# Kernel optimization log

Measured on AMD Instinct MI355X. Metric: run time of the kernel, lower is better.

Reference implementation:

```python
import jax, jax.numpy as jnp
import numpy as np

EPS = 1e-5
BANDLIMIT = 0.5
STEP_SCALE = 1.0


def _ln(x, g, b):
    mu = jnp.mean(x, axis=-1, keepdims=True)
    var = jnp.mean(jnp.square(x - mu), axis=-1, keepdims=True)
    return (x - mu) * jax.lax.rsqrt(var + EPS) * g + b


def _s5(u, Lambda_re, Lambda_im, B_re, B_im, C_re, C_im, D, log_step):
    # u: [N, T, C]; diagonal S5 SSM with ZOH discretization and parallel scan.
    Lam = Lambda_re + 1j * Lambda_im                      # [P] complex
    Bm = B_re + 1j * B_im                                  # [P, C]
    Cm = C_re + 1j * C_im                                  # [C, P]
    step = STEP_SCALE * jnp.exp(log_step)                  # [P]
    Lam_bar = jnp.exp(Lam * step)                          # [P]
    B_bar = ((Lam_bar - 1.0) / Lam)[:, None] * Bm          # [P, C]
    # bandlimit mask on output projection (freqs use un-scaled step)
    freqs = jnp.exp(log_step) * jnp.abs(Lambda_im) / (2.0 * jnp.pi)
    Cm = Cm * jnp.where(freqs < BANDLIMIT * 0.5, 1.0, 0.0)[None, :]
    Bu = jnp.einsum('ntc,pc->ntp', u.astype(B_bar.dtype), B_bar)  # [N,T,P] complex
    A = jnp.broadcast_to(Lam_bar, Bu.shape)

    def op(e1, e2):
        a1, b1 = e1
        a2, b2 = e2
        return a2 * a1, a2 * b1 + b2

    _, xs = jax.lax.associative_scan(op, (A, Bu), axis=1)   # x_t = Lam_bar*x_{t-1} + B_bar u_t (x_0 = 0)
    y = jnp.einsum('ntp,cp->ntc', xs, Cm).real + u * D
    return y


def setup_inputs() -> dict:
    key = jax.random.key(0)
    ks = jax.random.split(key, 16)
    B, T, H, W = 2, 15, 192, 192
    C, P = 16, 16
    sC = 1.0 / np.sqrt(C)
    sP = 1.0 / np.sqrt(P)
    inp = {}
    inp['x'] = jax.random.normal(ks[0], (B, T, H, W), dtype=jnp.float32)
    # input_proj: Linear(1, C)
    inp['w_in'] = jax.random.normal(ks[1], (C,), dtype=jnp.float32)
    inp['b_in'] = jnp.zeros((C,), dtype=jnp.float32)
    # S5Block attn_norm
    inp['attn_gamma'] = jnp.ones((C,), dtype=jnp.float32)
    inp['attn_beta'] = jnp.zeros((C,), dtype=jnp.float32)
    # S5 SSM parameters (stable: Re(Lambda) < 0)
    inp['Lambda_re'] = -jax.random.uniform(ks[2], (P,), jnp.float32, 0.1, 1.0)
    inp['Lambda_im'] = jnp.pi * jnp.arange(P, dtype=jnp.float32)
    inp['B_re'] = sC * jax.random.normal(ks[3], (P, C), dtype=jnp.float32)
    inp['B_im'] = sC * jax.random.normal(ks[4], (P, C), dtype=jnp.float32)
    inp['C_re'] = sP * jax.random.normal(ks[5], (C, P), dtype=jnp.float32)
    inp['C_im'] = sP * jax.random.normal(ks[6], (C, P), dtype=jnp.float32)
    inp['D'] = jax.random.normal(ks[7], (C,), dtype=jnp.float32)
    inp['log_step'] = jax.random.uniform(ks[8], (P,), jnp.float32, np.log(1e-3), np.log(0.1))
    # S5Block FFN (GEGLU, ff_mult=1.0, no bias)
    inp['ff_gamma'] = jnp.ones((C,), dtype=jnp.float32)
    inp['ff_beta'] = jnp.zeros((C,), dtype=jnp.float32)
    inp['W_enc'] = sC * jax.random.normal(ks[9], (2 * C, C), dtype=jnp.float32)
    inp['W_dec'] = sC * jax.random.normal(ks[10], (C, C), dtype=jnp.float32)
    # output_proj: LayerNorm(C) + Linear(C, C)
    inp['out_gamma'] = jnp.ones((C,), dtype=jnp.float32)
    inp['out_beta'] = jnp.zeros((C,), dtype=jnp.float32)
    inp['W_out'] = sC * jax.random.normal(ks[11], (C, C), dtype=jnp.float32)
    inp['b_out'] = jnp.zeros((C,), dtype=jnp.float32)
    return inp


def reference(x, w_in, b_in, attn_gamma, attn_beta, Lambda_re, Lambda_im,
              B_re, B_im, C_re, C_im, D, log_step,
              ff_gamma, ff_beta, W_enc, W_dec,
              out_gamma, out_beta, W_out, b_out):
    b, t, h, w = x.shape
    C = w_in.shape[0]
    # (b t h w) -> (b h w) t 1 -> Linear(1, C)
    u = jnp.transpose(x, (0, 2, 3, 1)).reshape(b * h * w, t)          # [N, T]
    u = u[:, :, None] * w_in + b_in                                     # [N, T, C]
    # --- S5Block ---
    fx = _ln(u, attn_gamma, attn_beta)
    s5_out = _s5(fx, Lambda_re, Lambda_im, B_re, B_im, C_re, C_im, D, log_step)
    z = jax.nn.gelu(s5_out, approximate=False) + fx
    fx2 = _ln(z, ff_gamma, ff_beta)
    enc = fx2 @ W_enc.T                                                 # [N, T, 2C]
    a, g = enc[..., :C], enc[..., C:]
    z2 = (a * jax.nn.gelu(g, approximate=False)) @ W_dec.T + fx2
    # aggregation = 'last'
    agg = z2[:, -1, :]                                                  # [N, C]
    # output_proj
    out = _ln(agg, out_gamma, out_beta) @ W_out.T + b_out               # [N, C]
    y = jnp.transpose(out.reshape(b, h, w, C), (0, 3, 1, 2))            # [B, C, H, W]
    return y
```

## Files before the change

### kernel.cpp

```cpp
#include <hip/hip_runtime.h>
#include <math.h>

#define HW_TOT 36864
#define T_LEN  15
#define NSEQ   73728
#define NBLK   576

#define OFF_F1    4
#define OFF_F2    20
#define OFF_F3    36
#define OFF_D     52
#define OFF_G3    68
#define OFF_G12   84
#define OFF_WENC  596
#define OFF_WDEC  1108
#define OFF_WOUT  1364
#define OFF_FFG   1620
#define OFF_FFB   1636
#define OFF_OG    1652
#define OFF_OB    1668
#define OFF_BOUT  1684
#define SM_N      1700

__device__ __forceinline__ float gelu_exact(float x){
  float ax = fabsf(x) * 0.7071067811865476f;
  float t  = 1.0f / (1.0f + 0.3275911f * ax);
  float poly = t*(0.254829592f + t*(-0.284496736f + t*(1.421413741f +
               t*(-1.453152027f + t*1.061405429f))));
  float er = 1.0f - poly * __expf(-ax*ax);
  er = copysignf(er, x);
  return 0.5f * x * (1.0f + er);
}

__global__ void __launch_bounds__(64) ssm_setup(
    const float* __restrict__ w_in, const float* __restrict__ b_in,
    const float* __restrict__ ag,   const float* __restrict__ ab,
    const float* __restrict__ Lre,  const float* __restrict__ Lim,
    const float* __restrict__ Bre,  const float* __restrict__ Bim,
    const float* __restrict__ Cre,  const float* __restrict__ Cim,
    const float* __restrict__ Dv,   const float* __restrict__ ls,
    const float* __restrict__ ffg,  const float* __restrict__ ffb,
    const float* __restrict__ Wenc, const float* __restrict__ Wdec,
    const float* __restrict__ og,   const float* __restrict__ ob,
    const float* __restrict__ Wout, const float* __restrict__ bout,
    float* __restrict__ ws)
{
  __shared__ float U1r[240], U1i[240], U2r[240], U2i[240];
  __shared__ float Cr[256], Ci[256], Qr[16], Qi[16];
  const int tid = threadIdx.x;

  float mw = 0.f, mb = 0.f;
  for (int c = 0; c < 16; ++c){ mw += w_in[c]; mb += b_in[c]; }
  mw *= 0.0625f; mb *= 0.0625f;
  float Saa = 0.f, Sad = 0.f, Sdd = 0.f;
  for (int c = 0; c < 16; ++c){
    float a = w_in[c]-mw, d = b_in[c]-mb;
    Saa += a*a; Sad += a*d; Sdd += d*d;
  }
  Saa *= 0.0625f; Sad *= 0.0625f; Sdd *= 0.0625f;
  if (tid == 0){ ws[0]=Saa; ws[1]=2.f*Sad; ws[2]=Sdd; ws[3]=0.f; }

  if (tid < 16){
    int c = tid;
    float a = w_in[c]-mw, d = b_in[c]-mb, g = ag[c];
    ws[OFF_F1+c] = a*g;
    ws[OFF_F2+c] = d*g;
    ws[OFF_F3+c] = ab[c];
    ws[OFF_D +c] = Dv[c];
    ws[OFF_FFG+c] = ffg[c];
    ws[OFF_FFB+c] = ffb[c];
    ws[OFF_OG +c] = og[c];
    ws[OFF_OB +c] = ob[c];
    ws[OFF_BOUT+c] = bout[c];
  }

  if (tid < 16){
    int p = tid;
    float step = expf(ls[p]);
    float lr = Lre[p], li = Lim[p];
    float er = expf(lr*step);
    float th = li*step;
    float Lbr = er*cosf(th), Lbi = er*sinf(th);
    float inv = 1.f/(lr*lr + li*li);
    float gr = Lbr - 1.f, gi = Lbi;
    float fr = (gr*lr + gi*li)*inv;
    float fi = (gi*lr - gr*li)*inv;
    float P1r=0,P1i=0,P2r=0,P2i=0,P3r=0,P3i=0;
    for (int c = 0; c < 16; ++c){
      float br = Bre[p*16+c], bi = Bim[p*16+c];
      float Bbr = fr*br - fi*bi, Bbi = fr*bi + fi*br;
      float a = w_in[c]-mw, d = b_in[c]-mb, g = ag[c];
      float f1 = a*g, f2 = d*g, f3 = ab[c];
      P1r += f1*Bbr; P1i += f1*Bbi;
      P2r += f2*Bbr; P2i += f2*Bbi;
      P3r += f3*Bbr; P3i += f3*Bbi;
    }
    float c1r=P1r, c1i=P1i, c2r=P2r, c2i=P2i;
    U1r[p*15+0]=c1r; U1i[p*15+0]=c1i;
    U2r[p*15+0]=c2r; U2i[p*15+0]=c2i;
    float kr=1.f, ki=0.f, pr=1.f, pi=0.f;
    for (int j = 1; j < T_LEN; ++j){
      float t1r = c1r*Lbr - c1i*Lbi, t1i = c1r*Lbi + c1i*Lbr;
      c1r=t1r; c1i=t1i;
      U1r[p*15+j]=c1r; U1i[p*15+j]=c1i;
      float t2r = c2r*Lbr - c2i*Lbi, t2i = c2r*Lbi + c2i*Lbr;
      c2r=t2r; c2i=t2i;
      U2r[p*15+j]=c2r; U2i[p*15+j]=c2i;
      float tpr = pr*Lbr - pi*Lbi, tpi = pr*Lbi + pi*Lbr;
      pr=tpr; pi=tpi;
      kr += pr; ki += pi;
    }
    Qr[p] = P3r*kr - P3i*ki;
    Qi[p] = P3r*ki + P3i*kr;
  }

  for (int k = tid; k < 256; k += 64){
    int p = k & 15;
    float step = expf(ls[p]);
    float freq = step * fabsf(Lim[p]) * 0.15915494309189535f;
    float m = (freq < 0.25f) ? 1.f : 0.f;
    Cr[k] = Cre[k]*m;
    Ci[k] = Cim[k]*m;
  }
  for (int k = tid; k < 512; k += 64) ws[OFF_WENC+k] = Wenc[k];
  for (int k = tid; k < 256; k += 64) ws[OFF_WDEC+k] = Wdec[k];
  for (int k = tid; k < 256; k += 64) ws[OFF_WOUT+k] = Wout[k];

  __syncthreads();

  for (int idx = tid; idx < 240; idx += 64){
    int c = idx / 15, t = idx - 15*c, j = 14 - t;
    float g1 = 0.f, g2 = 0.f;
    for (int p = 0; p < 16; ++p){
      float cr = Cr[c*16+p], ci = Ci[c*16+p];
      g1 = fmaf(cr, U1r[p*15+j], fmaf(-ci, U1i[p*15+j], g1));
      g2 = fmaf(cr, U2r[p*15+j], fmaf(-ci, U2i[p*15+j], g2));
    }
    ws[OFF_G12 + c*32 + 2*t    ] = g1;
    ws[OFF_G12 + c*32 + 2*t + 1] = g2;
  }
  if (tid < 16){
    int c = tid;
    float g3 = 0.f;
    for (int p = 0; p < 16; ++p)
      g3 = fmaf(Cr[c*16+p], Qr[p], fmaf(-Ci[c*16+p], Qi[p], g3));
    ws[OFF_G3+c] = g3;
  }
}

__global__ void __launch_bounds__(64) ssm_main(
    const float* __restrict__ x, const float* __restrict__ ws,
    float* __restrict__ out)
{
  __shared__ float sm[SM_N];
  const int tid = threadIdx.x;

  const int n0 = blockIdx.x * 128 + tid;
  const int n1 = n0 + 64;
  const int b0 = (n0 >= HW_TOT) ? 1 : 0;
  const int b1 = (n1 >= HW_TOT) ? 1 : 0;
  const int r0 = n0 - b0 * HW_TOT;
  const int r1 = n1 - b1 * HW_TOT;

  const float* xp0 = x + (size_t)b0 * (T_LEN * HW_TOT) + r0;
  const float* xp1 = x + (size_t)b1 * (T_LEN * HW_TOT) + r1;
  float xv[2][T_LEN];
#pragma unroll
  for (int t = 0; t < T_LEN; ++t){
    xv[0][t] = xp0[(size_t)t * HW_TOT];
    xv[1][t] = xp1[(size_t)t * HW_TOT];
  }

  for (int k = tid; k < SM_N; k += 64) sm[k] = ws[k];
  __syncthreads();

  const float Saa = sm[0], Sad2 = sm[1], Sdd = sm[2];
  float s1v[2][T_LEN], rsv[2][T_LEN];
#pragma unroll
  for (int s = 0; s < 2; ++s)
#pragma unroll
    for (int t = 0; t < T_LEN; ++t){
      float xt   = xv[s][t];
      float var  = fmaf(xt, fmaf(xt, Saa, Sad2), Sdd);
      float rstd = rsqrtf(var + 1e-5f);
      rsv[s][t] = rstd;
      s1v[s][t] = rstd * xt;
    }

  float z[2][16];
#pragma unroll
  for (int c = 0; c < 16; ++c){
    float a0 = sm[OFF_G3+c], a1 = a0;
#pragma unroll
    for (int t = 0; t < T_LEN; ++t){
      float g1 = sm[OFF_G12 + c*32 + 2*t];
      float g2 = sm[OFF_G12 + c*32 + 2*t + 1];
      a0 = fmaf(s1v[0][t], g1, fmaf(rsv[0][t], g2, a0));
      a1 = fmaf(s1v[1][t], g1, fmaf(rsv[1][t], g2, a1));
    }
    z[0][c] = a0; z[1][c] = a1;
  }

  float fx[2][16];
#pragma unroll
  for (int s = 0; s < 2; ++s){
    const float s1L = s1v[s][T_LEN-1], rsL = rsv[s][T_LEN-1];
#pragma unroll
    for (int c = 0; c < 16; ++c){
      float f = fmaf(s1L, sm[OFF_F1+c], fmaf(rsL, sm[OFF_F2+c], sm[OFF_F3+c]));
      fx[s][c] = f;
      float y = fmaf(f, sm[OFF_D+c], z[s][c]);
      z[s][c] = gelu_exact(y) + f;
    }
  }

  float fx2[2][16];
#pragma unroll
  for (int s = 0; s < 2; ++s){
    float mu = 0.f;
#pragma unroll
    for (int c = 0; c < 16; ++c) mu += z[s][c];
    mu *= 0.0625f;
    float vr = 0.f;
#pragma unroll
    for (int c = 0; c < 16; ++c){ float d = z[s][c]-mu; vr = fmaf(d,d,vr); }
    vr *= 0.0625f;
    float rs = rsqrtf(vr + 1e-5f);
#pragma unroll
    for (int c = 0; c < 16; ++c)
      fx2[s][c] = fmaf((z[s][c]-mu)*rs, sm[OFF_FFG+c], sm[OFF_FFB+c]);
  }

  float hg[2][16];
#pragma unroll
  for (int c = 0; c < 16; ++c){
    float a0=0.f, g0=0.f, a1=0.f, g1=0.f;
#pragma unroll
    for (int k = 0; k < 16; ++k){
      float wa = sm[OFF_WENC + c*16 + k];
      float wg = sm[OFF_WENC + (16+c)*16 + k];
      a0 = fmaf(fx2[0][k], wa, a0); g0 = fmaf(fx2[0][k], wg, g0);
      a1 = fmaf(fx2[1][k], wa, a1); g1 = fmaf(fx2[1][k], wg, g1);
    }
    hg[0][c] = a0 * gelu_exact(g0);
    hg[1][c] = a1 * gelu_exact(g1);
  }

  float z2[2][16];
#pragma unroll
  for (int c = 0; c < 16; ++c){
    float acc0 = fx2[0][c], acc1 = fx2[1][c];
#pragma unroll
    for (int k = 0; k < 16; ++k){
      float wd = sm[OFF_WDEC + c*16 + k];
      acc0 = fmaf(hg[0][k], wd, acc0);
      acc1 = fmaf(hg[1][k], wd, acc1);
    }
    z2[0][c] = acc0; z2[1][c] = acc1;
  }

  float qv[2][16];
#pragma unroll
  for (int s = 0; s < 2; ++s){
    float mu = 0.f;
#pragma unroll
    for (int c = 0; c < 16; ++c) mu += z2[s][c];
    mu *= 0.0625f;
    float vr = 0.f;
#pragma unroll
    for (int c = 0; c < 16; ++c){ float d = z2[s][c]-mu; vr = fmaf(d,d,vr); }
    vr *= 0.0625f;
    float rs = rsqrtf(vr + 1e-5f);
#pragma unroll
    for (int c = 0; c < 16; ++c)
      qv[s][c] = fmaf((z2[s][c]-mu)*rs, sm[OFF_OG+c], sm[OFF_OB+c]);
  }

  float* op0 = out + (size_t)b0 * (16*HW_TOT) + r0;
  float* op1 = out + (size_t)b1 * (16*HW_TOT) + r1;
#pragma unroll
  for (int c = 0; c < 16; ++c){
    float acc0 = sm[OFF_BOUT+c], acc1 = acc0;
#pragma unroll
    for (int k = 0; k < 16; ++k){
      float wo = sm[OFF_WOUT + c*16 + k];
      acc0 = fmaf(qv[0][k], wo, acc0);
      acc1 = fmaf(qv[1][k], wo, acc1);
    }
    op0[(size_t)c * HW_TOT] = acc0;
    op1[(size_t)c * HW_TOT] = acc1;
  }
}

extern "C" void kernel_launch(void* const* d_in, const int* in_sizes, int n_in,
                              void* d_out, int out_size, void* d_ws, size_t ws_size,
                              hipStream_t stream)
{
  const float* x    = (const float*)d_in[0];
  const float* w_in = (const float*)d_in[1];
  const float* b_in = (const float*)d_in[2];
  const float* ag   = (const float*)d_in[3];
  const float* ab   = (const float*)d_in[4];
  const float* Lre  = (const float*)d_in[5];
  const float* Lim  = (const float*)d_in[6];
  const float* Bre  = (const float*)d_in[7];
  const float* Bim  = (const float*)d_in[8];
  const float* Cre  = (const float*)d_in[9];
  const float* Cim  = (const float*)d_in[10];
  const float* Dv   = (const float*)d_in[11];
  const float* ls   = (const float*)d_in[12];
  const float* ffg  = (const float*)d_in[13];
  const float* ffb  = (const float*)d_in[14];
  const float* Wenc = (const float*)d_in[15];
  const float* Wdec = (const float*)d_in[16];
  const float* og   = (const float*)d_in[17];
  const float* ob   = (const float*)d_in[18];
  const float* Wout = (const float*)d_in[19];
  const float* bout = (const float*)d_in[20];
  float* ws  = (float*)d_ws;
  float* out = (float*)d_out;

  ssm_setup<<<1, 64, 0, stream>>>(w_in, b_in, ag, ab, Lre, Lim, Bre, Bim,
                                  Cre, Cim, Dv, ls, ffg, ffb, Wenc, Wdec,
                                  og, ob, Wout, bout, ws);
  ssm_main<<<NBLK, 64, 0, stream>>>(x, ws, out);
}
```

Baseline: 118.4 us.

## Fuse parameter setup kernel into main kernel, recomputing per block

Merges the single-block setup kernel into the main kernel. Each block now loads the raw parameters into shared memory and recomputes the folded SSM kernel coefficients (G12, G3, F123) itself, with no workspace round trip. This removes one kernel launch and the serialized single-block setup on the critical path. In exchange every block repeats the setup maths (exp, sin and cos, small matmuls), adds barriers and uses more shared memory per block, which may lower occupancy.

```diff
diff --git a/kernel.cpp b/kernel.cpp
--- a/kernel.cpp
+++ b/kernel.cpp
@@ -3,24 +3,29 @@
 
 #define HW_TOT 36864
 #define T_LEN  15
-#define NSEQ   73728
 #define NBLK   576
 
-#define OFF_F1    4
-#define OFF_F2    20
-#define OFF_F3    36
-#define OFF_D     52
-#define OFF_G3    68
-#define OFF_G12   84
-#define OFF_WENC  596
-#define OFF_WDEC  1108
-#define OFF_WOUT  1364
-#define OFF_FFG   1620
-#define OFF_FFB   1636
-#define OFF_OG    1652
-#define OFF_OB    1668
-#define OFF_BOUT  1684
-#define SM_N      1700
+#define R_WIN   0
+#define R_BIN   16
+#define R_AG    32
+#define R_AB    48
+#define R_LRE   64
+#define R_LIM   80
+#define R_LS    96
+#define R_DV    112
+#define R_FFG   128
+#define R_FFB   144
+#define R_OG    160
+#define R_OB    176
+#define R_BOUT  192
+#define R_BRE   208
+#define R_BIM   464
+#define R_CRE   720
+#define R_CIM   976
+#define R_WENC  1232
+#define R_WDEC  1744
+#define R_WOUT  2000
+#define R_N     2256
 
 __device__ __forceinline__ float gelu_exact(float x){
   float ax = fabsf(x) * 0.7071067811865476f;
@@ -32,7 +37,8 @@
   return 0.5f * x * (1.0f + er);
 }
 
-__global__ void __launch_bounds__(64) ssm_setup(
+__global__ void __launch_bounds__(64) ssm_fused(
+    const float* __restrict__ x,
     const float* __restrict__ w_in, const float* __restrict__ b_in,
     const float* __restrict__ ag,   const float* __restrict__ ab,
     const float* __restrict__ Lre,  const float* __restrict__ Lim,
@@ -43,41 +49,75 @@
     const float* __restrict__ Wenc, const float* __restrict__ Wdec,
     const float* __restrict__ og,   const float* __restrict__ ob,
     const float* __restrict__ Wout, const float* __restrict__ bout,
-    float* __restrict__ ws)
+    float* __restrict__ out)
 {
+  __shared__ float raw[R_N];
+  __shared__ float cmr[256], cmi[256];
   __shared__ float U1r[240], U1i[240], U2r[240], U2i[240];
-  __shared__ float Cr[256], Ci[256], Qr[16], Qi[16];
+  __shared__ float Qr[16], Qi[16];
+  __shared__ float G12[512];
+  __shared__ float G3[16];
+  __shared__ float F123[48];
+
   const int tid = threadIdx.x;
 
+  const int n0 = blockIdx.x * 128 + tid;
+  const int n1 = n0 + 64;
+  const int b0 = (n0 >= HW_TOT) ? 1 : 0;
+  const int b1 = (n1 >= HW_TOT) ? 1 : 0;
+  const int r0 = n0 - b0 * HW_TOT;
+  const int r1 = n1 - b1 * HW_TOT;
+  const float* xp0 = x + (size_t)b0 * (T_LEN * HW_TOT) + r0;
+  const float* xp1 = x + (size_t)b1 * (T_LEN * HW_TOT) + r1;
+  float xv[2][T_LEN];
+#pragma unroll
+  for (int t = 0; t < T_LEN; ++t){
+    xv[0][t] = xp0[(size_t)t * HW_TOT];
+    xv[1][t] = xp1[(size_t)t * HW_TOT];
+  }
+
+  if (tid < 16){
+    raw[R_WIN +tid] = w_in[tid];  raw[R_BIN +tid] = b_in[tid];
+    raw[R_AG  +tid] = ag[tid];    raw[R_AB  +tid] = ab[tid];
+    raw[R_LRE +tid] = Lre[tid];   raw[R_LIM +tid] = Lim[tid];
+    raw[R_LS  +tid] = ls[tid];    raw[R_DV  +tid] = Dv[tid];
+    raw[R_FFG +tid] = ffg[tid];   raw[R_FFB +tid] = ffb[tid];
+    raw[R_OG  +tid] = og[tid];    raw[R_OB  +tid] = ob[tid];
+    raw[R_BOUT+tid] = bout[tid];
+  }
+  for (int k = tid; k < 256; k += 64){
+    raw[R_BRE+k] = Bre[k]; raw[R_BIM+k] = Bim[k];
+    raw[R_CRE+k] = Cre[k]; raw[R_CIM+k] = Cim[k];
+  }
+  for (int k = tid; k < 512; k += 64) raw[R_WENC+k] = Wenc[k];
+  for (int k = tid; k < 256; k += 64){
+    raw[R_WDEC+k] = Wdec[k]; raw[R_WOUT+k] = Wout[k];
+  }
+  __syncthreads();
+
   float mw = 0.f, mb = 0.f;
-  for (int c = 0; c < 16; ++c){ mw += w_in[c]; mb += b_in[c]; }
+#pragma unroll
+  for (int c = 0; c < 16; ++c){ mw += raw[R_WIN+c]; mb += raw[R_BIN+c]; }
   mw *= 0.0625f; mb *= 0.0625f;
   float Saa = 0.f, Sad = 0.f, Sdd = 0.f;
-  for (int c = 0; c < 16; ++c){
-    float a = w_in[c]-mw, d = b_in[c]-mb;
-    Saa += a*a; Sad += a*d; Sdd += d*d;
-  }
-  Saa *= 0.0625f; Sad *= 0.0625f; Sdd *= 0.0625f;
-  if (tid == 0){ ws[0]=Saa; ws[1]=2.f*Sad; ws[2]=Sdd; ws[3]=0.f; }
+#pragma unroll
+  for (int c = 0; c < 16; ++c){
+    float a = raw[R_WIN+c]-mw, d = raw[R_BIN+c]-mb;
+    Saa = fmaf(a,a,Saa); Sad = fmaf(a,d,Sad); Sdd = fmaf(d,d,Sdd);
+  }
+  Saa *= 0.0625f; Sdd *= 0.0625f;
+  const float Sad2 = 2.f * Sad * 0.0625f;
 
   if (tid < 16){
-    int c = tid;
-    float a = w_in[c]-mw, d = b_in[c]-mb, g = ag[c];
-    ws[OFF_F1+c] = a*g;
-    ws[OFF_F2+c] = d*g;
-    ws[OFF_F3+c] = ab[c];
-    ws[OFF_D +c] = Dv[c];
-    ws[OFF_FFG+c] = ffg[c];
-    ws[OFF_FFB+c] = ffb[c];
-    ws[OFF_OG +c] = og[c];
-    ws[OFF_OB +c] = ob[c];
-    ws[OFF_BOUT+c] = bout[c];
-  }
-
-  if (tid < 16){
-    int p = tid;
-    float step = expf(ls[p]);
-    float lr = Lre[p], li = Lim[p];
+    const int p = tid;
+    {
+      float a = raw[R_WIN+p]-mw, d = raw[R_BIN+p]-mb, g = raw[R_AG+p];
+      F123[p]    = a*g;
+      F123[16+p] = d*g;
+      F123[32+p] = raw[R_AB+p];
+    }
+    float step = expf(raw[R_LS+p]);
+    float lr = raw[R_LRE+p], li = raw[R_LIM+p];
     float er = expf(lr*step);
     float th = li*step;
     float Lbr = er*cosf(th), Lbi = er*sinf(th);
@@ -87,13 +127,13 @@
     float fi = (gi*lr - gr*li)*inv;
     float P1r=0,P1i=0,P2r=0,P2i=0,P3r=0,P3i=0;
     for (int c = 0; c < 16; ++c){
-      float br = Bre[p*16+c], bi = Bim[p*16+c];
+      float br = raw[R_BRE+p*16+c], bi = raw[R_BIM+p*16+c];
       float Bbr = fr*br - fi*bi, Bbi = fr*bi + fi*br;
-      float a = w_in[c]-mw, d = b_in[c]-mb, g = ag[c];
-      float f1 = a*g, f2 = d*g, f3 = ab[c];
-      P1r += f1*Bbr; P1i += f1*Bbi;
-      P2r += f2*Bbr; P2i += f2*Bbi;
-      P3r += f3*Bbr; P3i += f3*Bbi;
+      float a = raw[R_WIN+c]-mw, d = raw[R_BIN+c]-mb, g = raw[R_AG+c];
+      float f1 = a*g, f2 = d*g, f3 = raw[R_AB+c];
+      P1r = fmaf(f1,Bbr,P1r); P1i = fmaf(f1,Bbi,P1i);
+      P2r = fmaf(f2,Bbr,P2r); P2i = fmaf(f2,Bbi,P2i);
+      P3r = fmaf(f3,Bbr,P3r); P3i = fmaf(f3,Bbi,P3i);
     }
     float c1r=P1r, c1i=P1i, c2r=P2r, c2i=P2i;
     U1r[p*15+0]=c1r; U1i[p*15+0]=c1i;
@@ -116,65 +156,34 @@
 
   for (int k = tid; k < 256; k += 64){
     int p = k & 15;
-    float step = expf(ls[p]);
-    float freq = step * fabsf(Lim[p]) * 0.15915494309189535f;
+    float step = expf(raw[R_LS+p]);
+    float freq = step * fabsf(raw[R_LIM+p]) * 0.15915494309189535f;
     float m = (freq < 0.25f) ? 1.f : 0.f;
-    Cr[k] = Cre[k]*m;
-    Ci[k] = Cim[k]*m;
-  }
-  for (int k = tid; k < 512; k += 64) ws[OFF_WENC+k] = Wenc[k];
-  for (int k = tid; k < 256; k += 64) ws[OFF_WDEC+k] = Wdec[k];
-  for (int k = tid; k < 256; k += 64) ws[OFF_WOUT+k] = Wout[k];
-
+    cmr[k] = raw[R_CRE+k]*m;
+    cmi[k] = raw[R_CIM+k]*m;
+  }
   __syncthreads();
 
   for (int idx = tid; idx < 240; idx += 64){
     int c = idx / 15, t = idx - 15*c, j = 14 - t;
     float g1 = 0.f, g2 = 0.f;
     for (int p = 0; p < 16; ++p){
-      float cr = Cr[c*16+p], ci = Ci[c*16+p];
+      float cr = cmr[c*16+p], ci = cmi[c*16+p];
       g1 = fmaf(cr, U1r[p*15+j], fmaf(-ci, U1i[p*15+j], g1));
       g2 = fmaf(cr, U2r[p*15+j], fmaf(-ci, U2i[p*15+j], g2));
     }
-    ws[OFF_G12 + c*32 + 2*t    ] = g1;
-    ws[OFF_G12 + c*32 + 2*t + 1] = g2;
+    G12[c*32 + 2*t    ] = g1;
+    G12[c*32 + 2*t + 1] = g2;
   }
   if (tid < 16){
     int c = tid;
     float g3 = 0.f;
     for (int p = 0; p < 16; ++p)
-      g3 = fmaf(Cr[c*16+p], Qr[p], fmaf(-Ci[c*16+p], Qi[p], g3));
-    ws[OFF_G3+c] = g3;
-  }
-}
-
-__global__ void __launch_bounds__(64) ssm_main(
-    const float* __restrict__ x, const float* __restrict__ ws,
-    float* __restrict__ out)
-{
-  __shared__ float sm[SM_N];
-  const int tid = threadIdx.x;
-
-  const int n0 = blockIdx.x * 128 + tid;
-  const int n1 = n0 + 64;
-  const int b0 = (n0 >= HW_TOT) ? 1 : 0;
-  const int b1 = (n1 >= HW_TOT) ? 1 : 0;
-  const int r0 = n0 - b0 * HW_TOT;
-  const int r1 = n1 - b1 * HW_TOT;
-
-  const float* xp0 = x + (size_t)b0 * (T_LEN * HW_TOT) + r0;
-  const float* xp1 = x + (size_t)b1 * (T_LEN * HW_TOT) + r1;
-  float xv[2][T_LEN];
-#pragma unroll
-  for (int t = 0; t < T_LEN; ++t){
-    xv[0][t] = xp0[(size_t)t * HW_TOT];
-    xv[1][t] = xp1[(size_t)t * HW_TOT];
-  }
-
-  for (int k = tid; k < SM_N; k += 64) sm[k] = ws[k];
+      g3 = fmaf(cmr[c*16+p], Qr[p], fmaf(-cmi[c*16+p], Qi[p], g3));
+    G3[c] = g3;
+  }
   __syncthreads();
 
-  const float Saa = sm[0], Sad2 = sm[1], Sdd = sm[2];
   float s1v[2][T_LEN], rsv[2][T_LEN];
 #pragma unroll
   for (int s = 0; s < 2; ++s)
@@ -190,33 +199,27 @@
   float z[2][16];
 #pragma unroll
   for (int c = 0; c < 16; ++c){
-    float a0 = sm[OFF_G3+c], a1 = a0;
+    float a0 = G3[c], a1 = a0;
 #pragma unroll
     for (int t = 0; t < T_LEN; ++t){
-      float g1 = sm[OFF_G12 + c*32 + 2*t];
-      float g2 = sm[OFF_G12 + c*32 + 2*t + 1];
+      float g1 = G12[c*32 + 2*t];
+      float g2 = G12[c*32 + 2*t + 1];
       a0 = fmaf(s1v[0][t], g1, fmaf(rsv[0][t], g2, a0));
       a1 = fmaf(s1v[1][t], g1, fmaf(rsv[1][t], g2, a1));
     }
     z[0][c] = a0; z[1][c] = a1;
   }
 
-  float fx[2][16];
+  float fx2[2][16];
 #pragma unroll
   for (int s = 0; s < 2; ++s){
     const float s1L = s1v[s][T_LEN-1], rsL = rsv[s][T_LEN-1];
 #pragma unroll
     for (int c = 0; c < 16; ++c){
-      float f = fmaf(s1L, sm[OFF_F1+c], fmaf(rsL, sm[OFF_F2+c], sm[OFF_F3+c]));
-      fx[s][c] = f;
-      float y = fmaf(f, sm[OFF_D+c], z[s][c]);
+      float f = fmaf(s1L, F123[c], fmaf(rsL, F123[16+c], F123[32+c]));
+      float y = fmaf(f, raw[R_DV+c], z[s][c]);
       z[s][c] = gelu_exact(y) + f;
     }
-  }
-
-  float fx2[2][16];
-#pragma unroll
-  for (int s = 0; s < 2; ++s){
     float mu = 0.f;
 #pragma unroll
     for (int c = 0; c < 16; ++c) mu += z[s][c];
@@ -228,7 +231,7 @@
     float rs = rsqrtf(vr + 1e-5f);
 #pragma unroll
     for (int c = 0; c < 16; ++c)
-      fx2[s][c] = fmaf((z[s][c]-mu)*rs, sm[OFF_FFG+c], sm[OFF_FFB+c]);
+      fx2[s][c] = fmaf((z[s][c]-mu)*rs, raw[R_FFG+c], raw[R_FFB+c]);
   }
 
   float hg[2][16];
@@ -237,8 +240,8 @@
     float a0=0.f, g0=0.f, a1=0.f, g1=0.f;
 #pragma unroll
     for (int k = 0; k < 16; ++k){
-      float wa = sm[OFF_WENC + c*16 + k];
-      float wg = sm[OFF_WENC + (16+c)*16 + k];
+      float wa = raw[R_WENC + c*16 + k];
+      float wg = raw[R_WENC + (16+c)*16 + k];
       a0 = fmaf(fx2[0][k], wa, a0); g0 = fmaf(fx2[0][k], wg, g0);
       a1 = fmaf(fx2[1][k], wa, a1); g1 = fmaf(fx2[1][k], wg, g1);
     }
@@ -252,7 +255,7 @@
     float acc0 = fx2[0][c], acc1 = fx2[1][c];
 #pragma unroll
     for (int k = 0; k < 16; ++k){
-      float wd = sm[OFF_WDEC + c*16 + k];
+      float wd = raw[R_WDEC + c*16 + k];
       acc0 = fmaf(hg[0][k], wd, acc0);
       acc1 = fmaf(hg[1][k], wd, acc1);
     }
@@ -273,17 +276,17 @@
     float rs = rsqrtf(vr + 1e-5f);
 #pragma unroll
     for (int c = 0; c < 16; ++c)
-      qv[s][c] = fmaf((z2[s][c]-mu)*rs, sm[OFF_OG+c], sm[OFF_OB+c]);
+      qv[s][c] = fmaf((z2[s][c]-mu)*rs, raw[R_OG+c], raw[R_OB+c]);
   }
 
   float* op0 = out + (size_t)b0 * (16*HW_TOT) + r0;
   float* op1 = out + (size_t)b1 * (16*HW_TOT) + r1;
 #pragma unroll
   for (int c = 0; c < 16; ++c){
-    float acc0 = sm[OFF_BOUT+c], acc1 = acc0;
+    float acc0 = raw[R_BOUT+c], acc1 = acc0;
 #pragma unroll
     for (int k = 0; k < 16; ++k){
-      float wo = sm[OFF_WOUT + c*16 + k];
+      float wo = raw[R_WOUT + c*16 + k];
       acc0 = fmaf(qv[0][k], wo, acc0);
       acc1 = fmaf(qv[1][k], wo, acc1);
     }
@@ -317,11 +320,9 @@
   const float* ob   = (const float*)d_in[18];
   const float* Wout = (const float*)d_in[19];
   const float* bout = (const float*)d_in[20];
-  float* ws  = (float*)d_ws;
   float* out = (float*)d_out;
 
-  ssm_setup<<<1, 64, 0, stream>>>(w_in, b_in, ag, ab, Lre, Lim, Bre, Bim,
-                                  Cre, Cim, Dv, ls, ffg, ffb, Wenc, Wdec,
-                                  og, ob, Wout, bout, ws);
-  ssm_main<<<NBLK, 64, 0, stream>>>(x, ws, out);
+  ssm_fused<<<NBLK, 64, 0, stream>>>(x, w_in, b_in, ag, ab, Lre, Lim,
+                                     Bre, Bim, Cre, Cim, Dv, ls, ffg, ffb,
+                                     Wenc, Wdec, og, ob, Wout, bout, out);
 }
```

Measured after the change: 119.0 us. No clear change (+0.5%).
